# Optimization experiments

Hardware: AMD Instinct MI355X
Metric: run time of the kernel (lower is better)

Reference implementation:

```python
import jax, jax.numpy as jnp
import numpy as np

WS = 15  # window_size


def setup_inputs() -> dict:
    key = jax.random.key(0)
    k1, k2, k3, k4 = jax.random.split(key, 4)
    x = jax.random.normal(k1, (4, 256, 200, 200), dtype=jnp.float32)
    theta_w = jax.random.normal(k2, (144, 256), dtype=jnp.float32) * 0.01
    phi_w = jax.random.normal(k3, (144, 256), dtype=jnp.float32) * 0.01
    # zero_init=False: use a small random projection so the output is nontrivial
    proj_w = jax.random.normal(k4, (256, 256), dtype=jnp.float32) * 0.01
    return {"x": x, "theta_w": theta_w, "phi_w": phi_w, "proj_w": proj_w}


def reference(x, theta_w, phi_w, proj_w):
    B, C, H, W = x.shape
    ws = WS
    pad_h = (ws - H % ws) % ws
    pad_w = (ws - W % ws) % ws
    xp = jnp.pad(x, ((0, 0), (0, 0), (0, pad_h), (0, pad_w)), mode='reflect')
    Hp, Wp = xp.shape[2], xp.shape[3]
    Nh, Nw = Hp // ws, Wp // ws
    # extract non-overlapping ws x ws windows -> (B*Nh*Nw, C, ws*ws)
    xw = (xp.reshape(B, C, Nh, ws, Nw, ws)
            .transpose(0, 2, 4, 1, 3, 5)
            .reshape(B * Nh * Nw, C, ws * ws))
    Ce = theta_w.shape[0]  # 144
    theta = jnp.einsum('ec,bcn->bne', theta_w, xw)   # (Bp, N, Ce)
    phi = jnp.einsum('ec,bcm->bem', phi_w, xw)       # (Bp, Ce, N)
    aff = jnp.einsum('bne,bem->bnm', theta, phi) / jnp.sqrt(jnp.asarray(Ce, x.dtype))
    aff = jax.nn.softmax(aff, axis=-1)               # (Bp, N, N)
    out = jnp.einsum('bnm,bcm->bcn', aff, xw)        # attention-weighted g (= x windows)
    out = jnp.einsum('oc,bcn->bon', proj_w, out)     # 1x1 projection
    # fold windows back -> (B, C, Hp, Wp), crop, residual
    y = (out.reshape(B, Nh, Nw, C, ws, ws)
            .transpose(0, 3, 1, 4, 2, 5)
            .reshape(B, C, Hp, Wp))
    y = y[:, :, :H, :W]
    return x + y
```

## Files before the change

kernel.cpp:

```cpp
#include <hip/hip_runtime.h>


#define WS_   15
#define B_    4
#define C_    256
#define H_    200
#define H2    (H_*H_)
#define NHW   14
#define NWIN  (B_*NHW*NHW)
#define NPOS  225
#define NWAVE 16

#define XT_STRIDE 264
#define PT_STRIDE 144
#define Z_STRIDE  240
#define TT_STRIDE 144
#define ST_STRIDE 240

#define XT_OFF    0
#define PT_OFF    59408
#define Z_OFF     93968
#define TT_OFF    155408
#define ST_OFF    157712
#define RMAX_OFF  161552
#define RSUM_OFF  162576
#define LDS_BYTES 163600

typedef __attribute__((ext_vector_type(4))) float floatx4;

__device__ inline unsigned char to_fp8(float v) {
    int r = __builtin_amdgcn_cvt_pk_fp8_f32(v, v, 0, false);
    return (unsigned char)(r & 0xFF);
}
__device__ inline long wfrag8(const float* p, float scale) {
    floatx4 a = *(const floatx4*)p;
    floatx4 b = *(const floatx4*)(p + 4);
    int lo = 0, hi = 0;
    lo = __builtin_amdgcn_cvt_pk_fp8_f32(a[0]*scale, a[1]*scale, lo, false);
    lo = __builtin_amdgcn_cvt_pk_fp8_f32(a[2]*scale, a[3]*scale, lo, true);
    hi = __builtin_amdgcn_cvt_pk_fp8_f32(b[0]*scale, b[1]*scale, hi, false);
    hi = __builtin_amdgcn_cvt_pk_fp8_f32(b[2]*scale, b[3]*scale, hi, true);
    return ((long)(unsigned)lo) | (((long)(unsigned)hi) << 32);
}
__device__ inline long ldsfrag(const char* p) { return *(const long*)p; }

#define MFMA8(a,b,c) __builtin_amdgcn_mfma_f32_16x16x32_fp8_fp8((a),(b),(c),0,0,0)

__device__ inline void bar_lds() {
    asm volatile("s_waitcnt lgkmcnt(0)" ::: "memory");
    __builtin_amdgcn_s_barrier();
}

__global__ __launch_bounds__(1024) void wnl_kernel(
    const float* __restrict__ x, const float* __restrict__ theta_w,
    const float* __restrict__ phi_w, const float* __restrict__ proj_w,
    float* __restrict__ out)
{
    __shared__ char lds[LDS_BYTES];
    char* XT = lds + XT_OFF;
    char* PT = lds + PT_OFF;
    char* Zs = lds + Z_OFF;
    char* TT = lds + TT_OFF;
    char* ST = lds + ST_OFF;
    float* rmaxf = (float*)(lds + RMAX_OFF);
    float* rsumf = (float*)(lds + RSUM_OFF);

    const int tid  = threadIdx.x;
    const int wv   = tid >> 6;
    const int lane = tid & 63;
    const int q    = lane >> 4;
    const int l16  = lane & 15;

    const int wid  = blockIdx.x;
    const int b    = wid / (NHW*NHW);
    const int rr   = wid % (NHW*NHW);
    const int row0 = (rr / NHW) * WS_;
    const int col0 = (rr % NHW) * WS_;
    const float* xb = x + (size_t)b * C_ * H2;

    long thw[8];
    long wA[8], wB[8];
    if (wv < 9) {
        const float* wrow = theta_w + (wv*16 + l16) * C_ + q*8;
        #pragma unroll
        for (int ck = 0; ck < 8; ++ck) thw[ck] = wfrag8(wrow + ck*32, 16.f);
    }
    {
        const float* wrowA = (wv < 9)
            ? (phi_w  + (wv*16     + l16) * C_ + q*8)
            : (proj_w + ((wv-9)*16 + l16) * C_ + q*8);
        #pragma unroll
        for (int ck = 0; ck < 8; ++ck) wA[ck] = wfrag8(wrowA + ck*32, 16.f);
        if (wv < 9) {
            const float* wrowB = proj_w + ((wv+7)*16 + l16) * C_ + q*8;
            #pragma unroll
            for (int ck = 0; ck < 8; ++ck) wB[ck] = wfrag8(wrowB + ck*32, 16.f);
        }
    }

    for (int idx = tid; idx < NPOS * C_; idx += 1024) {
        int c  = idx / NPOS;
        int n  = idx - c * NPOS;
        int wr = row0 + n / WS_;
        int wc = col0 + n % WS_;
        int gr = (wr < H_) ? wr : (2*H_ - 2 - wr);
        int gc = (wc < H_) ? wc : (2*H_ - 2 - wc);
        float v = xb[((size_t)c * H_ + gr) * H_ + gc];
        XT[n * XT_STRIDE + c] = (char)to_fp8(v);
    }
    if (tid < 16) rmaxf[tid*16 + 15] = -3.4e38f;
    bar_lds();

    if (wv < 9) {
        for (int mt = 0; mt < 15; ++mt) {
            floatx4 acc = {0.f,0.f,0.f,0.f};
            const char* arow = XT + (mt*16 + l16) * XT_STRIDE + q*8;
            #pragma unroll
            for (int ck = 0; ck < 8; ++ck)
                acc = MFMA8(ldsfrag(arow + ck*32), wA[ck], acc);
            #pragma unroll
            for (int r = 0; r < 4; ++r)
                PT[(mt*16 + q*4 + r) * PT_STRIDE + wv*16 + l16] = (char)to_fp8(acc[r]);
        }
        for (int mt = 0; mt < 15; ++mt) {
            floatx4 acc = {0.f,0.f,0.f,0.f};
            const char* brow = XT + (mt*16 + l16) * XT_STRIDE + q*8;
            #pragma unroll
            for (int ck = 0; ck < 8; ++ck)
                acc = MFMA8(wB[ck], ldsfrag(brow + ck*32), acc);
            int m = mt*16 + l16;
            #pragma unroll
            for (int r = 0; r < 4; ++r) {
                float v = (m < NPOS) ? acc[r] : 0.f;
                Zs[((wv+7)*16 + q*4 + r) * Z_STRIDE + m] = (char)to_fp8(v);
            }
        }
        {
            floatx4 acc = {0.f,0.f,0.f,0.f};
            const char* arow = XT + l16 * XT_STRIDE + q*8;
            #pragma unroll
            for (int ck = 0; ck < 8; ++ck)
                acc = MFMA8(ldsfrag(arow + ck*32), thw[ck], acc);
            #pragma unroll
            for (int r = 0; r < 4; ++r)
                TT[(q*4 + r) * TT_STRIDE + wv*16 + l16] = (char)to_fp8(acc[r]);
        }
    } else {
        const int ot = wv - 9;
        for (int mt = 0; mt < 15; ++mt) {
            floatx4 acc = {0.f,0.f,0.f,0.f};
            const char* brow = XT + (mt*16 + l16) * XT_STRIDE + q*8;
            #pragma unroll
            for (int ck = 0; ck < 8; ++ck)
                acc = MFMA8(wA[ck], ldsfrag(brow + ck*32), acc);
            int m = mt*16 + l16;
            #pragma unroll
            for (int r = 0; r < 4; ++r) {
                float v = (m < NPOS) ? acc[r] : 0.f;
                Zs[(ot*16 + q*4 + r) * Z_STRIDE + m] = (char)to_fp8(v);
            }
        }
    }
    bar_lds();

    for (int nt = 0; nt <= 15; ++nt) {
        const bool do_aff = (nt < 15);
        const bool do_pv  = (nt >= 1);

        float xr0=0.f, xr1=0.f, xr2=0.f, xr3=0.f;
        size_t gbase = 0; bool valid = false;
        if (do_pv) {
            const int n_o  = (nt-1)*16 + l16;
            const int wr_o = row0 + n_o / WS_;
            const int wc_o = col0 + n_o % WS_;
            valid = (n_o < NPOS) && (wr_o < H_) && (wc_o < H_);
            gbase = (((size_t)b * C_ + (wv*16 + q*4)) * H_ + wr_o) * H_ + wc_o;
            if (valid) {
                xr0 = x[gbase];
                xr1 = x[gbase + H2];
                xr2 = x[gbase + 2*(size_t)H2];
                xr3 = x[gbase + 3*(size_t)H2];
            }
        }

        floatx4 aacc = {0.f,0.f,0.f,0.f};
        if (do_aff) {
            long afr[5];
            const char* arow = TT + l16 * TT_STRIDE + q*8;
            #pragma unroll
            for (int kk = 0; kk < 4; ++kk) afr[kk] = ldsfrag(arow + kk*32);
            afr[4] = (q < 2) ? ldsfrag(TT + l16 * TT_STRIDE + 128 + q*8) : 0L;
            if (wv < 15) {
                const char* brow = PT + (wv*16 + l16) * PT_STRIDE + q*8;
                #pragma unroll
                for (int kk = 0; kk < 4; ++kk)
                    aacc = MFMA8(afr[kk], ldsfrag(brow + kk*32), aacc);
                long bf = (q < 2) ? ldsfrag(PT + (wv*16 + l16)*PT_STRIDE + 128 + q*8) : 0L;
                aacc = MFMA8(afr[4], bf, aacc);
                int m = wv*16 + l16;
                if (m >= NPOS) { aacc[0]=aacc[1]=aacc[2]=aacc[3] = -1e30f; }
                #pragma unroll
                for (int r = 0; r < 4; ++r) {
                    float v = aacc[r];
                    #pragma unroll
                    for (int off = 1; off < 16; off <<= 1) v = fmaxf(v, __shfl_xor(v, off));
                    if (l16 == 0) rmaxf[(q*4 + r)*16 + wv] = v;
                }
            }
        }

        if (do_pv) {
            float ssum = 0.f;
            #pragma unroll
            for (int w2 = 0; w2 < 15; ++w2) ssum += rsumf[w2*16 + l16];
            float sinv = 1.0f / (16.0f * ssum);
            long bfr[8];
            const char* srow = ST + l16 * ST_STRIDE + q*8;
            #pragma unroll
            for (int km = 0; km < 7; ++km) bfr[km] = ldsfrag(srow + km*32);
            bfr[7] = (q < 2) ? ldsfrag(ST + l16 * ST_STRIDE + 224 + q*8) : 0L;
            floatx4 acc = {0.f,0.f,0.f,0.f};
            const char* arow = Zs + (wv*16 + l16) * Z_STRIDE + q*8;
            #pragma unroll
            for (int km = 0; km < 7; ++km)
                acc = MFMA8(ldsfrag(arow + km*32), bfr[km], acc);
            long af = (q < 2) ? ldsfrag(Zs + (wv*16 + l16)*Z_STRIDE + 224 + q*8) : 0L;
            acc = MFMA8(af, bfr[7], acc);
            if (valid) {
                __builtin_nontemporal_store(xr0 + acc[0]*sinv, &out[gbase]);
                __builtin_nontemporal_store(xr1 + acc[1]*sinv, &out[gbase + H2]);
                __builtin_nontemporal_store(xr2 + acc[2]*sinv, &out[gbase + 2*(size_t)H2]);
                __builtin_nontemporal_store(xr3 + acc[3]*sinv, &out[gbase + 3*(size_t)H2]);
            }
        }

        if (do_aff) {
            bar_lds();

            if (wv < 15) {
                float gmax_[4];
                #pragma unroll
                for (int r = 0; r < 4; ++r) {
                    const floatx4* rm = (const floatx4*)(lds + RMAX_OFF + (q*4 + r)*64);
                    floatx4 aa = rm[0], bb = rm[1], cc = rm[2], dd = rm[3];
                    float g0 = fmaxf(fmaxf(aa[0],aa[1]), fmaxf(aa[2],aa[3]));
                    float g1 = fmaxf(fmaxf(bb[0],bb[1]), fmaxf(bb[2],bb[3]));
                    float g2 = fmaxf(fmaxf(cc[0],cc[1]), fmaxf(cc[2],cc[3]));
                    float g3 = fmaxf(fmaxf(dd[0],dd[1]), fmaxf(dd[2],dd[3]));
                    gmax_[r] = fmaxf(fmaxf(g0,g1), fmaxf(g2,g3));
                }
                float psum[4];
                #pragma unroll
                for (int r = 0; r < 4; ++r) {
                    float p = __expf((aacc[r] - gmax_[r]) * (1.0f/3072.0f));
                    ST[(q*4 + r) * ST_STRIDE + wv*16 + l16] = (char)to_fp8(p);
                    psum[r] = p;
                }
                #pragma unroll
                for (int r = 0; r < 4; ++r) {
                    float v = psum[r];
                    #pragma unroll
                    for (int off = 1; off < 16; off <<= 1) v += __shfl_xor(v, off);
                    if (l16 == 0) rsumf[wv*16 + q*4 + r] = v;
                }
            }
            if (wv < 9 && nt < 14) {
                floatx4 acc = {0.f,0.f,0.f,0.f};
                const char* arow = XT + ((nt+1)*16 + l16) * XT_STRIDE + q*8;
                #pragma unroll
                for (int ck = 0; ck < 8; ++ck)
                    acc = MFMA8(ldsfrag(arow + ck*32), thw[ck], acc);
                #pragma unroll
                for (int r = 0; r < 4; ++r)
                    TT[(q*4 + r) * TT_STRIDE + wv*16 + l16] = (char)to_fp8(acc[r]);
            }
            bar_lds();
        }
    }
}

extern "C" void kernel_launch(void* const* d_in, const int* in_sizes, int n_in,
                              void* d_out, int out_size, void* d_ws, size_t ws_size,
                              hipStream_t stream) {
    (void)in_sizes; (void)n_in; (void)out_size; (void)d_ws; (void)ws_size;
    const float* x   = (const float*)d_in[0];
    const float* tw  = (const float*)d_in[1];
    const float* pw  = (const float*)d_in[2];
    const float* prw = (const float*)d_in[3];
    wnl_kernel<<<NWIN, 1024, 0, stream>>>(x, tw, pw, prw, (float*)d_out);
}
```

Baseline: 767.9 us.

## Transpose MFMA operand order for packed fp8 stores and register-cached fragments

Swaps MFMA A/B operand roles so each lane holds four consecutive output elements along the stored dimension, allowing packed 4-byte fp8 stores instead of scattered byte stores for PT, Zs, TT and ST. It fuses the phi and proj-Z projections to share one set of XT fragment loads, and hoists the PT and Zs fragments into registers before the attention loop. It also restructures the window gather so each wave reads a channel with precomputed offsets, and simplifies the row max and sum reductions to two cross-lane shuffles. The cost is higher register pressure at 1024 threads per block, and the change drops the explicit initialization of the padding-wave rmax slot.

```diff
diff --git a/kernel.cpp b/kernel.cpp
--- a/kernel.cpp
+++ b/kernel.cpp
@@ -31,6 +31,10 @@
 __device__ inline unsigned char to_fp8(float v) {
     int r = __builtin_amdgcn_cvt_pk_fp8_f32(v, v, 0, false);
     return (unsigned char)(r & 0xFF);
+}
+__device__ inline int pack4(float a, float b, float c, float d) {
+    int pk = __builtin_amdgcn_cvt_pk_fp8_f32(a, b, 0, false);
+    return __builtin_amdgcn_cvt_pk_fp8_f32(c, d, pk, true);
 }
 __device__ inline long wfrag8(const float* p, float scale) {
     floatx4 a = *(const floatx4*)p;
@@ -98,70 +102,101 @@
         }
     }
 
-    for (int idx = tid; idx < NPOS * C_; idx += 1024) {
-        int c  = idx / NPOS;
-        int n  = idx - c * NPOS;
-        int wr = row0 + n / WS_;
-        int wc = col0 + n % WS_;
-        int gr = (wr < H_) ? wr : (2*H_ - 2 - wr);
-        int gc = (wc < H_) ? wc : (2*H_ - 2 - wc);
-        float v = xb[((size_t)c * H_ + gr) * H_ + gc];
-        XT[n * XT_STRIDE + c] = (char)to_fp8(v);
-    }
-    if (tid < 16) rmaxf[tid*16 + 15] = -3.4e38f;
+    {
+        int offg[4], offl[4];
+        bool okn[4];
+        #pragma unroll
+        for (int it = 0; it < 4; ++it) {
+            int n  = it*64 + lane;
+            okn[it] = (n < NPOS);
+            int nn = okn[it] ? n : 0;
+            int wr = row0 + nn / WS_;
+            int wc = col0 + nn % WS_;
+            int gr = (wr < H_) ? wr : (2*H_ - 2 - wr);
+            int gc = (wc < H_) ? wc : (2*H_ - 2 - wc);
+            offg[it] = gr * H_ + gc;
+            offl[it] = nn * XT_STRIDE;
+        }
+        for (int c = wv; c < C_; c += NWAVE) {
+            const float* xc = xb + (size_t)c * H2;
+            #pragma unroll
+            for (int it = 0; it < 4; ++it)
+                if (okn[it]) XT[offl[it] + c] = (char)to_fp8(xc[offg[it]]);
+        }
+    }
     bar_lds();
 
     if (wv < 9) {
         for (int mt = 0; mt < 15; ++mt) {
-            floatx4 acc = {0.f,0.f,0.f,0.f};
-            const char* arow = XT + (mt*16 + l16) * XT_STRIDE + q*8;
-            #pragma unroll
-            for (int ck = 0; ck < 8; ++ck)
-                acc = MFMA8(ldsfrag(arow + ck*32), wA[ck], acc);
-            #pragma unroll
-            for (int r = 0; r < 4; ++r)
-                PT[(mt*16 + q*4 + r) * PT_STRIDE + wv*16 + l16] = (char)to_fp8(acc[r]);
-        }
-        for (int mt = 0; mt < 15; ++mt) {
-            floatx4 acc = {0.f,0.f,0.f,0.f};
-            const char* brow = XT + (mt*16 + l16) * XT_STRIDE + q*8;
-            #pragma unroll
-            for (int ck = 0; ck < 8; ++ck)
-                acc = MFMA8(wB[ck], ldsfrag(brow + ck*32), acc);
-            int m = mt*16 + l16;
-            #pragma unroll
-            for (int r = 0; r < 4; ++r) {
-                float v = (m < NPOS) ? acc[r] : 0.f;
-                Zs[((wv+7)*16 + q*4 + r) * Z_STRIDE + m] = (char)to_fp8(v);
-            }
-        }
-        {
-            floatx4 acc = {0.f,0.f,0.f,0.f};
-            const char* arow = XT + l16 * XT_STRIDE + q*8;
-            #pragma unroll
-            for (int ck = 0; ck < 8; ++ck)
-                acc = MFMA8(ldsfrag(arow + ck*32), thw[ck], acc);
-            #pragma unroll
-            for (int r = 0; r < 4; ++r)
-                TT[(q*4 + r) * TT_STRIDE + wv*16 + l16] = (char)to_fp8(acc[r]);
+            long xf[8];
+            const char* xrow = XT + (mt*16 + l16) * XT_STRIDE + q*8;
+            #pragma unroll
+            for (int ck = 0; ck < 8; ++ck) xf[ck] = ldsfrag(xrow + ck*32);
+            floatx4 accP = {0.f,0.f,0.f,0.f};
+            floatx4 accZ = {0.f,0.f,0.f,0.f};
+            #pragma unroll
+            for (int ck = 0; ck < 8; ++ck) {
+                accP = MFMA8(wA[ck], xf[ck], accP);
+                accZ = MFMA8(xf[ck], wB[ck], accZ);
+            }
+            *(int*)(PT + (mt*16 + l16) * PT_STRIDE + wv*16 + 4*q) =
+                pack4(accP[0], accP[1], accP[2], accP[3]);
+            {
+                float z[4];
+                #pragma unroll
+                for (int r = 0; r < 4; ++r) {
+                    int m = mt*16 + 4*q + r;
+                    z[r] = (m < NPOS) ? accZ[r] : 0.f;
+                }
+                *(int*)(Zs + ((wv+7)*16 + l16) * Z_STRIDE + mt*16 + 4*q) =
+                    pack4(z[0], z[1], z[2], z[3]);
+            }
+            if (mt == 0) {
+                floatx4 accT = {0.f,0.f,0.f,0.f};
+                #pragma unroll
+                for (int ck = 0; ck < 8; ++ck)
+                    accT = MFMA8(thw[ck], xf[ck], accT);
+                *(int*)(TT + l16 * TT_STRIDE + wv*16 + 4*q) =
+                    pack4(accT[0], accT[1], accT[2], accT[3]);
+            }
         }
     } else {
         const int ot = wv - 9;
         for (int mt = 0; mt < 15; ++mt) {
-            floatx4 acc = {0.f,0.f,0.f,0.f};
-            const char* brow = XT + (mt*16 + l16) * XT_STRIDE + q*8;
+            long xf[8];
+            const char* xrow = XT + (mt*16 + l16) * XT_STRIDE + q*8;
+            #pragma unroll
+            for (int ck = 0; ck < 8; ++ck) xf[ck] = ldsfrag(xrow + ck*32);
+            floatx4 accZ = {0.f,0.f,0.f,0.f};
             #pragma unroll
             for (int ck = 0; ck < 8; ++ck)
-                acc = MFMA8(wA[ck], ldsfrag(brow + ck*32), acc);
-            int m = mt*16 + l16;
+                accZ = MFMA8(xf[ck], wA[ck], accZ);
+            float z[4];
             #pragma unroll
             for (int r = 0; r < 4; ++r) {
-                float v = (m < NPOS) ? acc[r] : 0.f;
-                Zs[(ot*16 + q*4 + r) * Z_STRIDE + m] = (char)to_fp8(v);
-            }
+                int m = mt*16 + 4*q + r;
+                z[r] = (m < NPOS) ? accZ[r] : 0.f;
+            }
+            *(int*)(Zs + (ot*16 + l16) * Z_STRIDE + mt*16 + 4*q) =
+                pack4(z[0], z[1], z[2], z[3]);
         }
     }
     bar_lds();
+
+    long pfr[5];
+    if (wv < 15) {
+        const char* prow = PT + (wv*16 + l16) * PT_STRIDE + q*8;
+        #pragma unroll
+        for (int kk = 0; kk < 4; ++kk) pfr[kk] = ldsfrag(prow + kk*32);
+        pfr[4] = (q < 2) ? ldsfrag(PT + (wv*16 + l16)*PT_STRIDE + 128 + q*8) : 0L;
+    }
+    long zfr[8];
+    {
+        const char* zrow = Zs + (wv*16 + l16) * Z_STRIDE + q*8;
+        #pragma unroll
+        for (int km = 0; km < 7; ++km) zfr[km] = ldsfrag(zrow + km*32);
+        zfr[7] = (q < 2) ? ldsfrag(Zs + (wv*16 + l16)*Z_STRIDE + 224 + q*8) : 0L;
+    }
 
     for (int nt = 0; nt <= 15; ++nt) {
         const bool do_aff = (nt < 15);
@@ -184,29 +219,26 @@
         }
 
         floatx4 aacc = {0.f,0.f,0.f,0.f};
-        if (do_aff) {
-            long afr[5];
-            const char* arow = TT + l16 * TT_STRIDE + q*8;
-            #pragma unroll
-            for (int kk = 0; kk < 4; ++kk) afr[kk] = ldsfrag(arow + kk*32);
-            afr[4] = (q < 2) ? ldsfrag(TT + l16 * TT_STRIDE + 128 + q*8) : 0L;
-            if (wv < 15) {
-                const char* brow = PT + (wv*16 + l16) * PT_STRIDE + q*8;
-                #pragma unroll
-                for (int kk = 0; kk < 4; ++kk)
-                    aacc = MFMA8(afr[kk], ldsfrag(brow + kk*32), aacc);
-                long bf = (q < 2) ? ldsfrag(PT + (wv*16 + l16)*PT_STRIDE + 128 + q*8) : 0L;
-                aacc = MFMA8(afr[4], bf, aacc);
-                int m = wv*16 + l16;
-                if (m >= NPOS) { aacc[0]=aacc[1]=aacc[2]=aacc[3] = -1e30f; }
-                #pragma unroll
-                for (int r = 0; r < 4; ++r) {
-                    float v = aacc[r];
-                    #pragma unroll
-                    for (int off = 1; off < 16; off <<= 1) v = fmaxf(v, __shfl_xor(v, off));
-                    if (l16 == 0) rmaxf[(q*4 + r)*16 + wv] = v;
-                }
-            }
+        if (do_aff && wv < 15) {
+            long tfr[5];
+            const char* trow = TT + l16 * TT_STRIDE + q*8;
+            #pragma unroll
+            for (int kk = 0; kk < 4; ++kk) tfr[kk] = ldsfrag(trow + kk*32);
+            tfr[4] = (q < 2) ? ldsfrag(TT + l16 * TT_STRIDE + 128 + q*8) : 0L;
+            #pragma unroll
+            for (int kk = 0; kk < 4; ++kk)
+                aacc = MFMA8(pfr[kk], tfr[kk], aacc);
+            aacc = MFMA8(pfr[4], tfr[4], aacc);
+            float vmax = -3.4e38f;
+            #pragma unroll
+            for (int r = 0; r < 4; ++r) {
+                int m = wv*16 + 4*q + r;
+                if (m >= NPOS) aacc[r] = -1e30f;
+                vmax = fmaxf(vmax, aacc[r]);
+            }
+            vmax = fmaxf(vmax, __shfl_xor(vmax, 16));
+            vmax = fmaxf(vmax, __shfl_xor(vmax, 32));
+            if (lane < 16) rmaxf[wv*16 + lane] = vmax;
         }
 
         if (do_pv) {
@@ -214,18 +246,16 @@
             #pragma unroll
             for (int w2 = 0; w2 < 15; ++w2) ssum += rsumf[w2*16 + l16];
             float sinv = 1.0f / (16.0f * ssum);
-            long bfr[8];
+            long sfr[8];
             const char* srow = ST + l16 * ST_STRIDE + q*8;
             #pragma unroll
-            for (int km = 0; km < 7; ++km) bfr[km] = ldsfrag(srow + km*32);
-            bfr[7] = (q < 2) ? ldsfrag(ST + l16 * ST_STRIDE + 224 + q*8) : 0L;
+            for (int km = 0; km < 7; ++km) sfr[km] = ldsfrag(srow + km*32);
+            sfr[7] = (q < 2) ? ldsfrag(ST + l16 * ST_STRIDE + 224 + q*8) : 0L;
             floatx4 acc = {0.f,0.f,0.f,0.f};
-            const char* arow = Zs + (wv*16 + l16) * Z_STRIDE + q*8;
             #pragma unroll
             for (int km = 0; km < 7; ++km)
-                acc = MFMA8(ldsfrag(arow + km*32), bfr[km], acc);
-            long af = (q < 2) ? ldsfrag(Zs + (wv*16 + l16)*Z_STRIDE + 224 + q*8) : 0L;
-            acc = MFMA8(af, bfr[7], acc);
+                acc = MFMA8(zfr[km], sfr[km], acc);
+            acc = MFMA8(zfr[7], sfr[7], acc);
             if (valid) {
                 __builtin_nontemporal_store(xr0 + acc[0]*sinv, &out[gbase]);
                 __builtin_nontemporal_store(xr1 + acc[1]*sinv, &out[gbase + H2]);
@@ -238,41 +268,28 @@
             bar_lds();
 
             if (wv < 15) {
-                float gmax_[4];
-                #pragma unroll
-                for (int r = 0; r < 4; ++r) {
-                    const floatx4* rm = (const floatx4*)(lds + RMAX_OFF + (q*4 + r)*64);
-                    floatx4 aa = rm[0], bb = rm[1], cc = rm[2], dd = rm[3];
-                    float g0 = fmaxf(fmaxf(aa[0],aa[1]), fmaxf(aa[2],aa[3]));
-                    float g1 = fmaxf(fmaxf(bb[0],bb[1]), fmaxf(bb[2],bb[3]));
-                    float g2 = fmaxf(fmaxf(cc[0],cc[1]), fmaxf(cc[2],cc[3]));
-                    float g3 = fmaxf(fmaxf(dd[0],dd[1]), fmaxf(dd[2],dd[3]));
-                    gmax_[r] = fmaxf(fmaxf(g0,g1), fmaxf(g2,g3));
-                }
-                float psum[4];
-                #pragma unroll
-                for (int r = 0; r < 4; ++r) {
-                    float p = __expf((aacc[r] - gmax_[r]) * (1.0f/3072.0f));
-                    ST[(q*4 + r) * ST_STRIDE + wv*16 + l16] = (char)to_fp8(p);
-                    psum[r] = p;
-                }
-                #pragma unroll
-                for (int r = 0; r < 4; ++r) {
-                    float v = psum[r];
-                    #pragma unroll
-                    for (int off = 1; off < 16; off <<= 1) v += __shfl_xor(v, off);
-                    if (l16 == 0) rsumf[wv*16 + q*4 + r] = v;
-                }
+                float g = rmaxf[l16];
+                #pragma unroll
+                for (int w2 = 1; w2 < 15; ++w2) g = fmaxf(g, rmaxf[w2*16 + l16]);
+                float p[4];
+                #pragma unroll
+                for (int r = 0; r < 4; ++r)
+                    p[r] = __expf((aacc[r] - g) * (1.0f/3072.0f));
+                *(int*)(ST + l16 * ST_STRIDE + wv*16 + 4*q) =
+                    pack4(p[0], p[1], p[2], p[3]);
+                float s = p[0] + p[1] + p[2] + p[3];
+                s += __shfl_xor(s, 16);
+                s += __shfl_xor(s, 32);
+                if (lane < 16) rsumf[wv*16 + lane] = s;
             }
             if (wv < 9 && nt < 14) {
-                floatx4 acc = {0.f,0.f,0.f,0.f};
-                const char* arow = XT + ((nt+1)*16 + l16) * XT_STRIDE + q*8;
+                floatx4 accT = {0.f,0.f,0.f,0.f};
+                const char* xrow = XT + ((nt+1)*16 + l16) * XT_STRIDE + q*8;
                 #pragma unroll
                 for (int ck = 0; ck < 8; ++ck)
-                    acc = MFMA8(ldsfrag(arow + ck*32), thw[ck], acc);
-                #pragma unroll
-                for (int r = 0; r < 4; ++r)
-                    TT[(q*4 + r) * TT_STRIDE + wv*16 + l16] = (char)to_fp8(acc[r]);
+                    accT = MFMA8(thw[ck], ldsfrag(xrow + ck*32), accT);
+                *(int*)(TT + l16 * TT_STRIDE + wv*16 + 4*q) =
+                    pack4(accT[0], accT[1], accT[2], accT[3]);
             }
             bar_lds();
         }
```

Result: faster. 645.6 us (-15.9%).
